# Optimization experiments

Hardware: AMD Instinct MI355X
Metric: run time of the kernel (lower is better)

Reference implementation:

```python
import jax, jax.numpy as jnp
import numpy as np

B, N, D = 2, 8192, 1024
H = 16
HD = D // H  # 64
EPS = 1e-6


def setup_inputs() -> dict:
    key = jax.random.key(0)
    ks = jax.random.split(key, 5)
    scale = 1.0 / np.sqrt(D)
    return {
        "x": jax.random.normal(ks[0], (B, N, D), dtype=jnp.float32),
        "Wq": jax.random.normal(ks[1], (D, D), dtype=jnp.float32) * scale,
        "Wk": jax.random.normal(ks[2], (D, D), dtype=jnp.float32) * scale,
        "Wv": jax.random.normal(ks[3], (D, D), dtype=jnp.float32) * scale,
        "Wo": jax.random.normal(ks[4], (D, D), dtype=jnp.float32) * scale,
    }


def _feature_map(a):
    # ELU + 1 (positive feature map)
    return jax.nn.elu(a) + 1.0


def reference(x, Wq, Wk, Wv, Wo):
    b, n, d = x.shape
    # torch nn.Linear: y = x @ W.T
    q = _feature_map((x @ Wq.T).reshape(b, n, H, HD))  # (B,N,H,hd)
    k = _feature_map((x @ Wk.T).reshape(b, n, H, HD))
    v = (x @ Wv.T).reshape(b, n, H, HD)
    # global kv state per head: (B,H,hd,hd)
    kv = jnp.einsum('bnhd,bnhm->bhdm', k, v)
    k_sum = k.sum(axis=1)  # (B,H,hd)
    numerator = jnp.einsum('bnhd,bhdm->bnhm', q, kv)  # (B,N,H,hd)
    denominator = jnp.einsum('bnhd,bhd->bnh', q, k_sum)[..., None]
    out = numerator / (denominator + EPS)
    out = out.reshape(b, n, d)
    return out @ Wo.T
```

## Files before the change

kernel.cpp:

```cpp
#include <hip/hip_runtime.h>
#include <stdint.h>

#define BB 2
#define NN 8192
#define DD 1024
#define KK 1024
#define NHEAD 16
#define HDIM 64
#define KV_CHUNKS 32

using f32x4  = __attribute__((ext_vector_type(4))) float;
using bf16x8 = __attribute__((ext_vector_type(8))) short;

__device__ __forceinline__ unsigned short f2bf(float f) {
  union { float f; unsigned int u; } v; v.f = f;
  unsigned int r = v.u + 0x7fffu + ((v.u >> 16) & 1u);
  return (unsigned short)(r >> 16);
}
__device__ __forceinline__ float bf2f(unsigned short u) {
  union { unsigned int u; float f; } v; v.u = ((unsigned int)u) << 16;
  return v.f;
}

__device__ __forceinline__ void gload_lds16(const unsigned short* g, unsigned short* l) {
  __builtin_amdgcn_global_load_lds(
      (__attribute__((address_space(1))) void*)(const_cast<unsigned short*>(g)),
      (__attribute__((address_space(3))) void*)(l), 16, 0, 0);
}

__global__ __launch_bounds__(256) void f32_to_bf16_k(const float* __restrict__ in,
                                                     unsigned short* __restrict__ out) {
  size_t i = ((size_t)blockIdx.x * 256 + threadIdx.x) * 8;
  float4 a = *(const float4*)(in + i);
  float4 b = *(const float4*)(in + i + 4);
  uint32_t p0 = (uint32_t)f2bf(a.x) | ((uint32_t)f2bf(a.y) << 16);
  uint32_t p1 = (uint32_t)f2bf(a.z) | ((uint32_t)f2bf(a.w) << 16);
  uint32_t p2 = (uint32_t)f2bf(b.x) | ((uint32_t)f2bf(b.y) << 16);
  uint32_t p3 = (uint32_t)f2bf(b.z) | ((uint32_t)f2bf(b.w) << 16);
  *(uint4*)(out + i) = make_uint4(p0, p1, p2, p3);
}

#define BAR  __builtin_amdgcn_s_barrier()
#define SB   __builtin_amdgcn_sched_barrier(0)
#define WLG  asm volatile("s_waitcnt lgkmcnt(0)" ::: "memory")
#define WVM4 asm volatile("s_waitcnt vmcnt(4)" ::: "memory")
#define WVM2 asm volatile("s_waitcnt vmcnt(2)" ::: "memory")
#define WVM0 asm volatile("s_waitcnt vmcnt(0)" ::: "memory")

__global__ __launch_bounds__(512, 2) void gemm256_qkv(const unsigned short* __restrict__ A,
                                                      const unsigned short* __restrict__ Bw,
                                                      unsigned short* __restrict__ O0,
                                                      unsigned short* __restrict__ O1,
                                                      unsigned short* __restrict__ O2) {
  __shared__ unsigned short lds[2][2][2][128 * 64];
  const int t = threadIdx.x;
  const int lane = t & 63;
  const int w = t >> 6;
  const int wm = w >> 2;
  const int wn = w & 3;
  const int frow = lane & 15;
  const int g = lane >> 4;
  const int fx = frow & 7;
  const int rowBase = blockIdx.x * 256;
  const int colBase = blockIdx.y * 256;

  const int srow0 = t >> 3;
  const int ssw = ((t & 7) ^ (srow0 & 7)) * 8;
  const unsigned short* sA0 = A + (size_t)(rowBase + srow0) * KK + ssw;
  const unsigned short* sA1 = A + (size_t)(rowBase + 64 + srow0) * KK + ssw;
  const unsigned short* sB0 = Bw + (size_t)(colBase + srow0) * KK + ssw;
  const unsigned short* sB1 = Bw + (size_t)(colBase + 64 + srow0) * KK + ssw;

#define STAGE(db, ab, half, kt)                                                        \
  do {                                                                                 \
    gload_lds16(((ab) ? sB0 : sA0) + (size_t)(half) * 128 * KK + (size_t)(kt) * 64,    \
                &lds[db][ab][half][(0 * 512 + w * 64) * 8]);                           \
    gload_lds16(((ab) ? sB1 : sA1) + (size_t)(half) * 128 * KK + (size_t)(kt) * 64,    \
                &lds[db][ab][half][(1 * 512 + w * 64) * 8]);                           \
  } while (0)

  bf16x8 ar[4][2], br[4][2];
  f32x4 acc[8][4];
#pragma unroll
  for (int i = 0; i < 8; ++i)
#pragma unroll
    for (int j = 0; j < 4; ++j) acc[i][j] = (f32x4){0.f, 0.f, 0.f, 0.f};

#define LDA4(db, mih)                                                                  \
  _Pragma("unroll") for (int mi2 = 0; mi2 < 4; ++mi2)                                  \
  _Pragma("unroll") for (int kk2 = 0; kk2 < 2; ++kk2)                                  \
    ar[mi2][kk2] = *(const bf16x8*)((const char*)&lds[db][0][wm][0] +                  \
        ((mih) * 64 + mi2 * 16 + frow) * 128 + ((kk2 * 4 + g) ^ fx) * 16);

#define LDB2(db, nih)                                                                  \
  _Pragma("unroll") for (int ni2 = 0; ni2 < 2; ++ni2)                                  \
  _Pragma("unroll") for (int kk2 = 0; kk2 < 2; ++kk2)                                  \
    br[(nih) * 2 + ni2][kk2] = *(const bf16x8*)((const char*)&lds[db][1][wn >> 1][0] + \
        ((wn & 1) * 64 + (nih) * 32 + ni2 * 16 + frow) * 128 + ((kk2 * 4 + g) ^ fx) * 16);

#define MFMAQ(mih, nih)                                                                \
  __builtin_amdgcn_s_setprio(1);                                                      \
  _Pragma("unroll") for (int mi2 = 0; mi2 < 4; ++mi2)                                  \
  _Pragma("unroll") for (int ni2 = 0; ni2 < 2; ++ni2)                                  \
  _Pragma("unroll") for (int kk2 = 0; kk2 < 2; ++kk2)                                  \
    acc[(mih) * 4 + mi2][(nih) * 2 + ni2] = __builtin_amdgcn_mfma_f32_16x16x32_bf16(   \
        ar[mi2][kk2], br[(nih) * 2 + ni2][kk2],                                        \
        acc[(mih) * 4 + mi2][(nih) * 2 + ni2], 0, 0, 0);                               \
  __builtin_amdgcn_s_setprio(0);

  STAGE(0, 1, 0, 0); STAGE(0, 1, 1, 0);
  STAGE(0, 0, 0, 0); STAGE(0, 0, 1, 0);
  STAGE(1, 1, 0, 1); STAGE(1, 1, 1, 1);
  WVM4; BAR; SB;

#pragma unroll 1
  for (int i = 0; i < 8; ++i) {
    const bool full = (i < 7);
    const int kt1 = 2 * i + 1, kt2 = 2 * i + 2, kt3 = 2 * i + 3;
    LDA4(0, 0); LDB2(0, 0);
    STAGE(1, 0, 0, kt1);
    BAR; WLG; SB; MFMAQ(0, 0); BAR; SB;
    LDB2(0, 1);
    STAGE(1, 0, 1, kt1);
    BAR; WLG; SB; MFMAQ(0, 1); BAR; SB;
    LDA4(0, 1);
    if (full) STAGE(0, 1, 0, kt2);
    BAR; WLG; SB; MFMAQ(1, 0); BAR; SB;
    if (full) { STAGE(0, 1, 1, kt2); WVM4; } else { WVM0; }
    BAR; SB; MFMAQ(1, 1); BAR; SB;
    LDA4(1, 0); LDB2(1, 0);
    if (full) STAGE(0, 0, 0, kt2);
    BAR; WLG; SB; MFMAQ(0, 0); BAR; SB;
    LDB2(1, 1);
    if (full) STAGE(0, 0, 1, kt2);
    BAR; WLG; SB; MFMAQ(0, 1); BAR; SB;
    LDA4(1, 1);
    if (full) STAGE(1, 1, 0, kt3);
    BAR; WLG; SB; MFMAQ(1, 0); BAR; SB;
    if (full) { STAGE(1, 1, 1, kt3); WVM4; }
    BAR; SB; MFMAQ(1, 1); BAR; SB;
  }

  const int r0 = rowBase + wm * 128 + g * 4;
  const int ymat = blockIdx.y >> 2;
  unsigned short* dst = (ymat == 0) ? O0 : ((ymat == 1) ? O1 : O2);
  const int c0 = (blockIdx.y & 3) * 256 + wn * 64 + frow;
  const bool doElu = (ymat < 2);
#pragma unroll
  for (int mi = 0; mi < 8; ++mi)
#pragma unroll
    for (int j = 0; j < 4; ++j) {
      const size_t ro = (size_t)(r0 + mi * 16 + j) * DD;
#pragma unroll
      for (int ni = 0; ni < 4; ++ni) {
        float v = acc[mi][ni][j];
        if (doElu) v = (v > 0.f) ? (v + 1.f) : __expf(v);
        dst[ro + c0 + ni * 16] = f2bf(v);
      }
    }
#undef STAGE
#undef LDA4
#undef LDB2
#undef MFMAQ
}

__global__ __launch_bounds__(256, 2) void gemm_bt_f32(const unsigned short* __restrict__ A,
                                                      const unsigned short* __restrict__ Bw,
                                                      float* __restrict__ Cp,
                                                      int M, int N, int K) {
  constexpr int BM = 128, BN = 128, BK = 64;
  __shared__ unsigned short As[BM * BK];
  __shared__ unsigned short Bs[BN * BK];
  const int t = threadIdx.x;
  const int lane = t & 63;
  const int w = t >> 6;
  const int wr = w >> 1, wc = w & 1;
  const int rowBase = blockIdx.x * BM;
  const int colBase = blockIdx.y * BN;

  f32x4 acc[4][4];
#pragma unroll
  for (int i = 0; i < 4; ++i)
#pragma unroll
    for (int j = 0; j < 4; ++j) acc[i][j] = (f32x4){0.f, 0.f, 0.f, 0.f};

  const int sr = t >> 3;
  const int sc = (t & 7) * 8;
  const unsigned short* gA = A + (size_t)(rowBase + sr) * K + sc;
  const unsigned short* gB = Bw + (size_t)(colBase + sr) * K + sc;

  for (int k0 = 0; k0 < K; k0 += BK) {
#pragma unroll
    for (int i = 0; i < 4; ++i) {
      gload_lds16(gA + (size_t)i * 32 * K + k0, As + (i * 256 + w * 64) * 8);
      gload_lds16(gB + (size_t)i * 32 * K + k0, Bs + (i * 256 + w * 64) * 8);
    }
    __syncthreads();
#pragma unroll
    for (int kk = 0; kk < BK; kk += 32) {
      bf16x8 af[4], bfv[4];
#pragma unroll
      for (int mi = 0; mi < 4; ++mi)
        af[mi] = *(const bf16x8*)(As + (wr * 64 + mi * 16 + (lane & 15)) * BK + kk + (lane >> 4) * 8);
#pragma unroll
      for (int ni = 0; ni < 4; ++ni)
        bfv[ni] = *(const bf16x8*)(Bs + (wc * 64 + ni * 16 + (lane & 15)) * BK + kk + (lane >> 4) * 8);
#pragma unroll
      for (int mi = 0; mi < 4; ++mi)
#pragma unroll
        for (int ni = 0; ni < 4; ++ni)
          acc[mi][ni] = __builtin_amdgcn_mfma_f32_16x16x32_bf16(af[mi], bfv[ni], acc[mi][ni], 0, 0, 0);
    }
    __syncthreads();
  }

  const int r0 = rowBase + wr * 64 + ((lane >> 4) << 2);
  const int c0 = colBase + wc * 64 + (lane & 15);
#pragma unroll
  for (int mi = 0; mi < 4; ++mi)
#pragma unroll
    for (int j = 0; j < 4; ++j) {
      const size_t rowOff = (size_t)(r0 + mi * 16 + j) * N;
#pragma unroll
      for (int ni = 0; ni < 4; ++ni)
        Cp[rowOff + c0 + ni * 16] = acc[mi][ni][j];
    }
}

__global__ __launch_bounds__(256) void kv_mfma(const unsigned short* __restrict__ Kb,
                                               const unsigned short* __restrict__ Vb,
                                               float* __restrict__ kvp,
                                               float* __restrict__ ksp) {
  __shared__ unsigned short kt[2][32 * 64];
  __shared__ unsigned short vt[2][32 * 64];
  const int blk = blockIdx.x;
  const int c = blk % KV_CHUNKS;
  const int h = (blk / KV_CHUNKS) % NHEAD;
  const int b = blk / (KV_CHUNKS * NHEAD);
  const int t = threadIdx.x;
  const int lane = t & 63;
  const int w = t >> 6;
  const int frow = lane & 15;
  const int g = lane >> 4;
  const int chunkLen = NN / KV_CHUNKS;
  const int NSTEP = chunkLen / 32;

  const size_t base = ((size_t)b * NN + (size_t)c * chunkLen) * DD + h * HDIM;
  const unsigned short* sK = Kb + base + (size_t)(t >> 3) * DD + (t & 7) * 8;
  const unsigned short* sV = Vb + base + (size_t)(t >> 3) * DD + (t & 7) * 8;

  bf16x8 ones;
#pragma unroll
  for (int j = 0; j < 8; ++j) ones[j] = (short)0x3F80;

  f32x4 acc[4], aks;
#pragma unroll
  for (int mt = 0; mt < 4; ++mt) acc[mt] = (f32x4){0.f, 0.f, 0.f, 0.f};
  aks = (f32x4){0.f, 0.f, 0.f, 0.f};

  gload_lds16(sK, &kt[0][t * 8]);
  gload_lds16(sV, &vt[0][t * 8]);

#pragma unroll 1
  for (int s = 0; s < NSTEP; ++s) {
    const int cur = s & 1;
    BAR;
    if (s + 1 < NSTEP) {
      gload_lds16(sK + (size_t)(s + 1) * 32 * DD, &kt[cur ^ 1][t * 8]);
      gload_lds16(sV + (size_t)(s + 1) * 32 * DD, &vt[cur ^ 1][t * 8]);
      WVM2;
    } else {
      WVM0;
    }
    BAR; SB;

    bf16x8 a;
#pragma unroll
    for (int j = 0; j < 8; ++j)
      a[j] = (short)kt[cur][(g * 8 + j) * 64 + w * 16 + frow];
#pragma unroll
    for (int mt = 0; mt < 4; ++mt) {
      bf16x8 bfr;
#pragma unroll
      for (int j = 0; j < 8; ++j)
        bfr[j] = (short)vt[cur][(g * 8 + j) * 64 + mt * 16 + frow];
      acc[mt] = __builtin_amdgcn_mfma_f32_16x16x32_bf16(a, bfr, acc[mt], 0, 0, 0);
    }
    aks = __builtin_amdgcn_mfma_f32_16x16x32_bf16(a, ones, aks, 0, 0, 0);
  }

  float* dst = kvp + (size_t)blk * 4096;
#pragma unroll
  for (int mt = 0; mt < 4; ++mt)
#pragma unroll
    for (int j = 0; j < 4; ++j)
      dst[(w * 16 + g * 4 + j) * 64 + mt * 16 + frow] = acc[mt][j];
  if (frow == 0) {
#pragma unroll
    for (int j = 0; j < 4; ++j)
      ksp[(size_t)blk * 64 + w * 16 + g * 4 + j] = aks[j];
  }
}

__global__ __launch_bounds__(256) void kv_final(const float* __restrict__ kvp,
                                                const float* __restrict__ ksp,
                                                unsigned short* __restrict__ kvb) {
  const int bh = blockIdx.x;
  const int t = threadIdx.x;
  __shared__ float kvs[4096];
#pragma unroll
  for (int e0 = 0; e0 < 4096; e0 += 256) {
    float s = 0.f;
    for (int cI = 0; cI < KV_CHUNKS; ++cI)
      s += kvp[((size_t)bh * KV_CHUNKS + cI) * 4096 + e0 + t];
    kvs[e0 + t] = s;
  }
  __syncthreads();
  unsigned short* dst = kvb + (size_t)bh * (96 * 64);
#pragma unroll
  for (int e0 = 0; e0 < 4096; e0 += 256) {
    int e = e0 + t;
    dst[e] = f2bf(kvs[(e & 63) * 64 + (e >> 6)]);
  }
  if (t < 64) {
    float s = 0.f;
    for (int cI = 0; cI < KV_CHUNKS; ++cI)
      s += ksp[((size_t)bh * KV_CHUNKS + cI) * 64 + t];
    dst[64 * 64 + t] = f2bf(s);
  }
  for (int e0 = 65 * 64; e0 < 96 * 64; e0 += 256) {
    int e = e0 + t;
    if (e < 96 * 64) dst[e] = 0;
  }
}

__global__ __launch_bounds__(256) void attn_mfma(const unsigned short* __restrict__ Qb,
                                                 const unsigned short* __restrict__ kvb,
                                                 unsigned short* __restrict__ Ob) {
  __shared__ unsigned short Bs[96 * 64];
  __shared__ unsigned short Qs[64 * 64];
  const int t = threadIdx.x;
  const int lane = t & 63;
  const int w = t >> 6;
  const int bh = blockIdx.y;
  const int b = bh >> 4;
  const int h = bh & 15;
  const int rowBase = blockIdx.x * 64;

  const unsigned short* bsrc = kvb + (size_t)bh * (96 * 64);
#pragma unroll
  for (int r = 0; r < 3; ++r) {
    int ci = r * 256 + t;
    int row = ci >> 3, ch = ci & 7;
    gload_lds16(bsrc + row * 64 + (ch ^ (row & 7)) * 8, Bs + ci * 8);
  }
  const int sr = t >> 3, ch0 = t & 7;
#pragma unroll
  for (int i = 0; i < 2; ++i) {
    int row = i * 32 + sr;
    const unsigned short* src =
        Qb + ((size_t)(b * NN + rowBase + row)) * DD + h * HDIM + (ch0 ^ (row & 7)) * 8;
    gload_lds16(src, Qs + row * 64 + ch0 * 8);
  }
  __syncthreads();

  const int frow = lane & 15;
  const int g = lane >> 4;
  bf16x8 a[2];
#pragma unroll
  for (int kk = 0; kk < 2; ++kk)
    a[kk] = *(const bf16x8*)(Qs + (w * 16 + frow) * 64 + ((kk * 4 + g) ^ (lane & 7)) * 8);

  f32x4 acc[5];
#pragma unroll
  for (int c = 0; c < 5; ++c) acc[c] = (f32x4){0.f, 0.f, 0.f, 0.f};
#pragma unroll
  for (int c = 0; c < 5; ++c) {
#pragma unroll
    for (int kk = 0; kk < 2; ++kk) {
      bf16x8 bf = *(const bf16x8*)(Bs + (c * 16 + frow) * 64 + ((kk * 4 + g) ^ (lane & 7)) * 8);
      acc[c] = __builtin_amdgcn_mfma_f32_16x16x32_bf16(a[kk], bf, acc[c], 0, 0, 0);
    }
  }

  float rden[4];
#pragma unroll
  for (int j = 0; j < 4; ++j) {
    float den = __shfl(acc[4][j], g * 16, 64);
    rden[j] = 1.f / (den + 1e-6f);
  }
  const size_t obase = ((size_t)(b * NN + rowBase + w * 16 + g * 4)) * DD + h * HDIM + frow;
#pragma unroll
  for (int c = 0; c < 4; ++c)
#pragma unroll
    for (int j = 0; j < 4; ++j)
      Ob[obase + (size_t)j * DD + c * 16] = f2bf(acc[c][j] * rden[j]);
}

extern "C" void kernel_launch(void* const* d_in, const int* in_sizes, int n_in,
                              void* d_out, int out_size, void* d_ws, size_t ws_size,
                              hipStream_t stream) {
  const float* x  = (const float*)d_in[0];
  const float* Wq = (const float*)d_in[1];
  const float* Wk = (const float*)d_in[2];
  const float* Wv = (const float*)d_in[3];
  const float* Wo = (const float*)d_in[4];
  float* out = (float*)d_out;

  char* ws = (char*)d_ws;
  size_t off = 0;
  auto alloc = [&](size_t bytes) -> char* {
    char* p = ws + off;
    off += (bytes + 255) & ~(size_t)255;
    return p;
  };
  const size_t xN = (size_t)BB * NN * DD;
  unsigned short* xb   = (unsigned short*)alloc(xN * 2);
  unsigned short* qb   = (unsigned short*)alloc(xN * 2);
  unsigned short* kb   = (unsigned short*)alloc(xN * 2);
  unsigned short* vb   = (unsigned short*)alloc(xN * 2);
  unsigned short* wqkv = (unsigned short*)alloc((size_t)3 * DD * DD * 2);
  unsigned short* wob  = (unsigned short*)alloc((size_t)DD * DD * 2);
  float* ksp = (float*)alloc((size_t)BB * NHEAD * KV_CHUNKS * 64 * 4);
  unsigned short* kvb = (unsigned short*)alloc((size_t)BB * NHEAD * 96 * 64 * 2);
  float* kvp = (float*)xb;
  unsigned short* ob = xb;

  f32_to_bf16_k<<<(int)(xN / (256 * 8)), 256, 0, stream>>>(x, xb);
  f32_to_bf16_k<<<(DD * DD) / (256 * 8), 256, 0, stream>>>(Wq, wqkv);
  f32_to_bf16_k<<<(DD * DD) / (256 * 8), 256, 0, stream>>>(Wk, wqkv + (size_t)DD * DD);
  f32_to_bf16_k<<<(DD * DD) / (256 * 8), 256, 0, stream>>>(Wv, wqkv + (size_t)2 * DD * DD);
  f32_to_bf16_k<<<(DD * DD) / (256 * 8), 256, 0, stream>>>(Wo, wob);

  dim3 gq(64, 12);
  gemm256_qkv<<<gq, 512, 0, stream>>>(xb, wqkv, qb, kb, vb);

  kv_mfma<<<BB * NHEAD * KV_CHUNKS, 256, 0, stream>>>(kb, vb, kvp, ksp);
  kv_final<<<BB * NHEAD, 256, 0, stream>>>(kvp, ksp, kvb);

  dim3 ga(NN / 64, BB * NHEAD);
  attn_mfma<<<ga, 256, 0, stream>>>(qb, kvb, ob);

  dim3 go(128, 8);
  gemm_bt_f32<<<go, 256, 0, stream>>>(ob, wob, out, BB * NN, DD, DD);
}
```

Before: 233.7 us.

## Reuse tuned 256-tile GEMM for output projection, fuse conversions, widen attention tiles

The output projection now uses the templated 256x256 pipelined GEMM, with an fp32 epilogue, in place of the simple unpipelined 128x128 kernel. The five fp32-to-bf16 conversion launches are merged into one kernel. The attention kernel handles 128 rows per block, so each kv tile loaded into LDS is reused twice. The vmcnt wait in the QKV GEMM moves after the MFMA so loads overlap more compute. In exchange the output GEMM runs only 256 blocks, which may leave CUs idle, and the conversion kernel gains per-thread branching.

```diff
diff --git a/kernel.cpp b/kernel.cpp
--- a/kernel.cpp
+++ b/kernel.cpp
@@ -28,30 +28,50 @@
       (__attribute__((address_space(3))) void*)(l), 16, 0, 0);
 }
 
-__global__ __launch_bounds__(256) void f32_to_bf16_k(const float* __restrict__ in,
-                                                     unsigned short* __restrict__ out) {
+__global__ __launch_bounds__(256) void convert_all(const float* __restrict__ x,
+                                                   const float* __restrict__ Wq,
+                                                   const float* __restrict__ Wk,
+                                                   const float* __restrict__ Wv,
+                                                   const float* __restrict__ Wo,
+                                                   unsigned short* __restrict__ xb,
+                                                   unsigned short* __restrict__ wqkv,
+                                                   unsigned short* __restrict__ wob) {
   size_t i = ((size_t)blockIdx.x * 256 + threadIdx.x) * 8;
-  float4 a = *(const float4*)(in + i);
-  float4 b = *(const float4*)(in + i + 4);
+  const size_t xN = (size_t)BB * NN * DD;
+  const float* src;
+  unsigned short* dst;
+  size_t off;
+  if (i < xN) {
+    src = x; dst = xb; off = i;
+  } else {
+    size_t r = i - xN;
+    int wsel = (int)(r >> 20);
+    off = r & 1048575;
+    src = (wsel == 0) ? Wq : (wsel == 1) ? Wk : (wsel == 2) ? Wv : Wo;
+    dst = (wsel < 3) ? (wqkv + (size_t)wsel * 1048576) : wob;
+  }
+  float4 a = *(const float4*)(src + off);
+  float4 b = *(const float4*)(src + off + 4);
   uint32_t p0 = (uint32_t)f2bf(a.x) | ((uint32_t)f2bf(a.y) << 16);
   uint32_t p1 = (uint32_t)f2bf(a.z) | ((uint32_t)f2bf(a.w) << 16);
   uint32_t p2 = (uint32_t)f2bf(b.x) | ((uint32_t)f2bf(b.y) << 16);
   uint32_t p3 = (uint32_t)f2bf(b.z) | ((uint32_t)f2bf(b.w) << 16);
-  *(uint4*)(out + i) = make_uint4(p0, p1, p2, p3);
+  *(uint4*)(dst + off) = make_uint4(p0, p1, p2, p3);
 }
 
 #define BAR  __builtin_amdgcn_s_barrier()
 #define SB   __builtin_amdgcn_sched_barrier(0)
 #define WLG  asm volatile("s_waitcnt lgkmcnt(0)" ::: "memory")
 #define WVM4 asm volatile("s_waitcnt vmcnt(4)" ::: "memory")
-#define WVM2 asm volatile("s_waitcnt vmcnt(2)" ::: "memory")
 #define WVM0 asm volatile("s_waitcnt vmcnt(0)" ::: "memory")
 
-__global__ __launch_bounds__(512, 2) void gemm256_qkv(const unsigned short* __restrict__ A,
-                                                      const unsigned short* __restrict__ Bw,
-                                                      unsigned short* __restrict__ O0,
-                                                      unsigned short* __restrict__ O1,
-                                                      unsigned short* __restrict__ O2) {
+template <int EPI>
+__global__ __launch_bounds__(512, 2) void gemm256(const unsigned short* __restrict__ A,
+                                                  const unsigned short* __restrict__ Bw,
+                                                  unsigned short* __restrict__ O0,
+                                                  unsigned short* __restrict__ O1,
+                                                  unsigned short* __restrict__ O2,
+                                                  float* __restrict__ OF) {
   __shared__ unsigned short lds[2][2][2][128 * 64];
   const int t = threadIdx.x;
   const int lane = t & 63;
@@ -126,8 +146,10 @@
     LDA4(0, 1);
     if (full) STAGE(0, 1, 0, kt2);
     BAR; WLG; SB; MFMAQ(1, 0); BAR; SB;
-    if (full) { STAGE(0, 1, 1, kt2); WVM4; } else { WVM0; }
-    BAR; SB; MFMAQ(1, 1); BAR; SB;
+    if (full) STAGE(0, 1, 1, kt2);
+    BAR; SB; MFMAQ(1, 1);
+    if (full) { WVM4; } else { WVM0; }
+    BAR; SB;
     LDA4(1, 0); LDB2(1, 0);
     if (full) STAGE(0, 0, 0, kt2);
     BAR; WLG; SB; MFMAQ(0, 0); BAR; SB;
@@ -137,94 +159,46 @@
     LDA4(1, 1);
     if (full) STAGE(1, 1, 0, kt3);
     BAR; WLG; SB; MFMAQ(1, 0); BAR; SB;
-    if (full) { STAGE(1, 1, 1, kt3); WVM4; }
-    BAR; SB; MFMAQ(1, 1); BAR; SB;
+    if (full) STAGE(1, 1, 1, kt3);
+    BAR; SB; MFMAQ(1, 1);
+    if (full) { WVM4; }
+    BAR; SB;
   }
 
   const int r0 = rowBase + wm * 128 + g * 4;
-  const int ymat = blockIdx.y >> 2;
-  unsigned short* dst = (ymat == 0) ? O0 : ((ymat == 1) ? O1 : O2);
-  const int c0 = (blockIdx.y & 3) * 256 + wn * 64 + frow;
-  const bool doElu = (ymat < 2);
-#pragma unroll
-  for (int mi = 0; mi < 8; ++mi)
-#pragma unroll
-    for (int j = 0; j < 4; ++j) {
-      const size_t ro = (size_t)(r0 + mi * 16 + j) * DD;
-#pragma unroll
-      for (int ni = 0; ni < 4; ++ni) {
-        float v = acc[mi][ni][j];
-        if (doElu) v = (v > 0.f) ? (v + 1.f) : __expf(v);
-        dst[ro + c0 + ni * 16] = f2bf(v);
+  if constexpr (EPI == 0) {
+    const int ymat = blockIdx.y >> 2;
+    unsigned short* dst = (ymat == 0) ? O0 : ((ymat == 1) ? O1 : O2);
+    const int c0 = (blockIdx.y & 3) * 256 + wn * 64 + frow;
+    const bool doElu = (ymat < 2);
+#pragma unroll
+    for (int mi = 0; mi < 8; ++mi)
+#pragma unroll
+      for (int j = 0; j < 4; ++j) {
+        const size_t ro = (size_t)(r0 + mi * 16 + j) * DD;
+#pragma unroll
+        for (int ni = 0; ni < 4; ++ni) {
+          float v = acc[mi][ni][j];
+          if (doElu) v = (v > 0.f) ? (v + 1.f) : __expf(v);
+          dst[ro + c0 + ni * 16] = f2bf(v);
+        }
       }
-    }
+  } else {
+    const int c0 = colBase + wn * 64 + frow;
+#pragma unroll
+    for (int mi = 0; mi < 8; ++mi)
+#pragma unroll
+      for (int j = 0; j < 4; ++j) {
+        const size_t ro = (size_t)(r0 + mi * 16 + j) * DD;
+#pragma unroll
+        for (int ni = 0; ni < 4; ++ni)
+          OF[ro + c0 + ni * 16] = acc[mi][ni][j];
+      }
+  }
 #undef STAGE
 #undef LDA4
 #undef LDB2
 #undef MFMAQ
-}
-
-__global__ __launch_bounds__(256, 2) void gemm_bt_f32(const unsigned short* __restrict__ A,
-                                                      const unsigned short* __restrict__ Bw,
-                                                      float* __restrict__ Cp,
-                                                      int M, int N, int K) {
-  constexpr int BM = 128, BN = 128, BK = 64;
-  __shared__ unsigned short As[BM * BK];
-  __shared__ unsigned short Bs[BN * BK];
-  const int t = threadIdx.x;
-  const int lane = t & 63;
-  const int w = t >> 6;
-  const int wr = w >> 1, wc = w & 1;
-  const int rowBase = blockIdx.x * BM;
-  const int colBase = blockIdx.y * BN;
-
-  f32x4 acc[4][4];
-#pragma unroll
-  for (int i = 0; i < 4; ++i)
-#pragma unroll
-    for (int j = 0; j < 4; ++j) acc[i][j] = (f32x4){0.f, 0.f, 0.f, 0.f};
-
-  const int sr = t >> 3;
-  const int sc = (t & 7) * 8;
-  const unsigned short* gA = A + (size_t)(rowBase + sr) * K + sc;
-  const unsigned short* gB = Bw + (size_t)(colBase + sr) * K + sc;
-
-  for (int k0 = 0; k0 < K; k0 += BK) {
-#pragma unroll
-    for (int i = 0; i < 4; ++i) {
-      gload_lds16(gA + (size_t)i * 32 * K + k0, As + (i * 256 + w * 64) * 8);
-      gload_lds16(gB + (size_t)i * 32 * K + k0, Bs + (i * 256 + w * 64) * 8);
-    }
-    __syncthreads();
-#pragma unroll
-    for (int kk = 0; kk < BK; kk += 32) {
-      bf16x8 af[4], bfv[4];
-#pragma unroll
-      for (int mi = 0; mi < 4; ++mi)
-        af[mi] = *(const bf16x8*)(As + (wr * 64 + mi * 16 + (lane & 15)) * BK + kk + (lane >> 4) * 8);
-#pragma unroll
-      for (int ni = 0; ni < 4; ++ni)
-        bfv[ni] = *(const bf16x8*)(Bs + (wc * 64 + ni * 16 + (lane & 15)) * BK + kk + (lane >> 4) * 8);
-#pragma unroll
-      for (int mi = 0; mi < 4; ++mi)
-#pragma unroll
-        for (int ni = 0; ni < 4; ++ni)
-          acc[mi][ni] = __builtin_amdgcn_mfma_f32_16x16x32_bf16(af[mi], bfv[ni], acc[mi][ni], 0, 0, 0);
-    }
-    __syncthreads();
-  }
-
-  const int r0 = rowBase + wr * 64 + ((lane >> 4) << 2);
-  const int c0 = colBase + wc * 64 + (lane & 15);
-#pragma unroll
-  for (int mi = 0; mi < 4; ++mi)
-#pragma unroll
-    for (int j = 0; j < 4; ++j) {
-      const size_t rowOff = (size_t)(r0 + mi * 16 + j) * N;
-#pragma unroll
-      for (int ni = 0; ni < 4; ++ni)
-        Cp[rowOff + c0 + ni * 16] = acc[mi][ni][j];
-    }
 }
 
 __global__ __launch_bounds__(256) void kv_mfma(const unsigned short* __restrict__ Kb,
@@ -268,7 +242,7 @@
     if (s + 1 < NSTEP) {
       gload_lds16(sK + (size_t)(s + 1) * 32 * DD, &kt[cur ^ 1][t * 8]);
       gload_lds16(sV + (size_t)(s + 1) * 32 * DD, &vt[cur ^ 1][t * 8]);
-      WVM2;
+      asm volatile("s_waitcnt vmcnt(2)" ::: "memory");
     } else {
       WVM0;
     }
@@ -338,14 +312,14 @@
                                                  const unsigned short* __restrict__ kvb,
                                                  unsigned short* __restrict__ Ob) {
   __shared__ unsigned short Bs[96 * 64];
-  __shared__ unsigned short Qs[64 * 64];
+  __shared__ unsigned short Qs[128 * 64];
   const int t = threadIdx.x;
   const int lane = t & 63;
   const int w = t >> 6;
   const int bh = blockIdx.y;
   const int b = bh >> 4;
   const int h = bh & 15;
-  const int rowBase = blockIdx.x * 64;
+  const int rowBase = blockIdx.x * 128;
 
   const unsigned short* bsrc = kvb + (size_t)bh * (96 * 64);
 #pragma unroll
@@ -356,7 +330,7 @@
   }
   const int sr = t >> 3, ch0 = t & 7;
 #pragma unroll
-  for (int i = 0; i < 2; ++i) {
+  for (int i = 0; i < 4; ++i) {
     int row = i * 32 + sr;
     const unsigned short* src =
         Qb + ((size_t)(b * NN + rowBase + row)) * DD + h * HDIM + (ch0 ^ (row & 7)) * 8;
@@ -366,35 +340,45 @@
 
   const int frow = lane & 15;
   const int g = lane >> 4;
-  bf16x8 a[2];
-#pragma unroll
-  for (int kk = 0; kk < 2; ++kk)
-    a[kk] = *(const bf16x8*)(Qs + (w * 16 + frow) * 64 + ((kk * 4 + g) ^ (lane & 7)) * 8);
-
-  f32x4 acc[5];
-#pragma unroll
-  for (int c = 0; c < 5; ++c) acc[c] = (f32x4){0.f, 0.f, 0.f, 0.f};
+  bf16x8 a[2][2];
+#pragma unroll
+  for (int rb = 0; rb < 2; ++rb)
+#pragma unroll
+    for (int kk = 0; kk < 2; ++kk)
+      a[rb][kk] = *(const bf16x8*)(Qs + (rb * 64 + w * 16 + frow) * 64 + ((kk * 4 + g) ^ (lane & 7)) * 8);
+
+  f32x4 acc[2][5];
+#pragma unroll
+  for (int rb = 0; rb < 2; ++rb)
+#pragma unroll
+    for (int c = 0; c < 5; ++c) acc[rb][c] = (f32x4){0.f, 0.f, 0.f, 0.f};
 #pragma unroll
   for (int c = 0; c < 5; ++c) {
 #pragma unroll
     for (int kk = 0; kk < 2; ++kk) {
       bf16x8 bf = *(const bf16x8*)(Bs + (c * 16 + frow) * 64 + ((kk * 4 + g) ^ (lane & 7)) * 8);
-      acc[c] = __builtin_amdgcn_mfma_f32_16x16x32_bf16(a[kk], bf, acc[c], 0, 0, 0);
+#pragma unroll
+      for (int rb = 0; rb < 2; ++rb)
+        acc[rb][c] = __builtin_amdgcn_mfma_f32_16x16x32_bf16(a[rb][kk], bf, acc[rb][c], 0, 0, 0);
     }
   }
 
-  float rden[4];
-#pragma unroll
-  for (int j = 0; j < 4; ++j) {
-    float den = __shfl(acc[4][j], g * 16, 64);
-    rden[j] = 1.f / (den + 1e-6f);
-  }
-  const size_t obase = ((size_t)(b * NN + rowBase + w * 16 + g * 4)) * DD + h * HDIM + frow;
-#pragma unroll
-  for (int c = 0; c < 4; ++c)
-#pragma unroll
-    for (int j = 0; j < 4; ++j)
-      Ob[obase + (size_t)j * DD + c * 16] = f2bf(acc[c][j] * rden[j]);
+#pragma unroll
+  for (int rb = 0; rb < 2; ++rb) {
+    float rden[4];
+#pragma unroll
+    for (int j = 0; j < 4; ++j) {
+      float den = __shfl(acc[rb][4][j], g * 16, 64);
+      rden[j] = 1.f / (den + 1e-6f);
+    }
+    const size_t obase =
+        ((size_t)(b * NN + rowBase + rb * 64 + w * 16 + g * 4)) * DD + h * HDIM + frow;
+#pragma unroll
+    for (int c = 0; c < 4; ++c)
+#pragma unroll
+      for (int j = 0; j < 4; ++j)
+        Ob[obase + (size_t)j * DD + c * 16] = f2bf(acc[rb][c][j] * rden[j]);
+  }
 }
 
 extern "C" void kernel_launch(void* const* d_in, const int* in_sizes, int n_in,
@@ -426,21 +410,18 @@
   float* kvp = (float*)xb;
   unsigned short* ob = xb;
 
-  f32_to_bf16_k<<<(int)(xN / (256 * 8)), 256, 0, stream>>>(x, xb);
-  f32_to_bf16_k<<<(DD * DD) / (256 * 8), 256, 0, stream>>>(Wq, wqkv);
-  f32_to_bf16_k<<<(DD * DD) / (256 * 8), 256, 0, stream>>>(Wk, wqkv + (size_t)DD * DD);
-  f32_to_bf16_k<<<(DD * DD) / (256 * 8), 256, 0, stream>>>(Wv, wqkv + (size_t)2 * DD * DD);
-  f32_to_bf16_k<<<(DD * DD) / (256 * 8), 256, 0, stream>>>(Wo, wob);
+  const int convBlocks = (int)((xN + 4 * 1048576) / 2048);
+  convert_all<<<convBlocks, 256, 0, stream>>>(x, Wq, Wk, Wv, Wo, xb, wqkv, wob);
 
   dim3 gq(64, 12);
-  gemm256_qkv<<<gq, 512, 0, stream>>>(xb, wqkv, qb, kb, vb);
+  gemm256<0><<<gq, 512, 0, stream>>>(xb, wqkv, qb, kb, vb, nullptr);
 
   kv_mfma<<<BB * NHEAD * KV_CHUNKS, 256, 0, stream>>>(kb, vb, kvp, ksp);
   kv_final<<<BB * NHEAD, 256, 0, stream>>>(kvp, ksp, kvb);
 
-  dim3 ga(NN / 64, BB * NHEAD);
+  dim3 ga(NN / 128, BB * NHEAD);
   attn_mfma<<<ga, 256, 0, stream>>>(qb, kvb, ob);
 
-  dim3 go(128, 8);
-  gemm_bt_f32<<<go, 256, 0, stream>>>(ob, wob, out, BB * NN, DD, DD);
-}
+  dim3 go(64, 4);
+  gemm256<1><<<go, 512, 0, stream>>>(ob, wob, nullptr, nullptr, nullptr, out);
+}
```

After: 207.3 us (median of 3 runs). 1.13x faster.
